# Performance work log

Measured on AMD Instinct MI355X. Metric: run time of the kernel, lower is better.

Reference implementation:

```python
import jax, jax.numpy as jnp
import numpy as np

ATT_K = 180   # attention_k
NPOOL = 15    # WeldonPooling(15): mean of top-15 + mean of bottom-15 spatial scores


def setup_inputs() -> dict:
    key = jax.random.key(0)
    k1, k2, k3, k4 = jax.random.split(key, 4)
    imgs, emb, h, w = 16, 2400, 14, 14
    caps_cnt = 64
    return {
        "g": jax.random.normal(k1, (imgs, emb, h, w), dtype=jnp.float32),
        "caps": jax.random.normal(k2, (caps_cnt, emb), dtype=jnp.float32),
        "fc_w": jax.random.normal(k3, (emb, emb), dtype=jnp.float32) * 0.02,
        "fc_b": jax.random.normal(k4, (emb,), dtype=jnp.float32) * 0.02,
    }


def reference(g, caps, fc_w, fc_b):
    imgs, emb, h, w = g.shape
    caps_cnt = caps.shape[0]

    # ---- WeldonPooling(15): per (img, channel) sort spatial scores ----
    flat = g.reshape(imgs, emb, h * w)
    s = jnp.sort(flat, axis=2)  # ascending
    hpool = s[:, :, -NPOOL:].mean(axis=2) + s[:, :, :NPOOL].mean(axis=2)  # [imgs, emb]
    x = hpool @ fc_w.T + fc_b  # fc (dropout is identity at eval / p=0)

    # ---- get_heat_map: top-k caption dims, gather fc-projected features ----
    order = jnp.argsort(-caps, axis=1)[:, :ATT_K]                 # [C, k] indices
    vals = jnp.take_along_axis(caps, order, axis=1)               # [C, k] top-k values (desc)
    gf = jnp.einsum('oe,iehw->oihw', fc_w, g)                     # fc.weight @ g -> [emb, imgs, h, w]
    gsel = gf[order]                                              # gather -> [C, k, imgs, h, w]
    heat = jnp.sum(jnp.abs(gsel * vals[:, :, None, None, None]), axis=1)  # [C, imgs, h, w]
    heat = jnp.transpose(heat, (1, 0, 2, 3))                      # [imgs, C, h, w]
    heat = heat / jnp.sum(heat, axis=(2, 3), keepdims=True)       # normalize per (img, cap)

    # ---- attention_embedding: weighted spatial sum, then fc ----
    xa = jnp.einsum('ichw,iehw->ice', heat, g)                    # [imgs, C, emb]
    xa = xa @ fc_w.T + fc_b

    return x, xa, g
```

## Files before the change

### kernel.cpp

```cpp
#include <hip/hip_runtime.h>
#include <math.h>

#define IMGS 16
#define EMB 2400
#define HW 196
#define CAPS 64
#define ATTK 180
#define NPOOL 15
#define NCOLS (IMGS * HW)
#define KPAD 224

typedef __attribute__((ext_vector_type(8))) short short8;
typedef __attribute__((ext_vector_type(4))) float f32x4;
typedef const __attribute__((address_space(1))) unsigned int* gas1_t;
typedef __attribute__((address_space(3))) unsigned int* las3_t;
typedef unsigned long long ull;

__device__ inline unsigned short f2bf(float f) {
    unsigned int u = __builtin_bit_cast(unsigned int, f);
    u += 0x7fffu + ((u >> 16) & 1u);
    return (unsigned short)(u >> 16);
}
__device__ inline float bf2f(unsigned int lo16) {
    return __builtin_bit_cast(float, lo16 << 16);
}
__device__ inline unsigned f2sort(float f) {
    unsigned u = __builtin_bit_cast(unsigned, f);
    int msk = ((int)u) >> 31;
    return u ^ (unsigned)(msk | 0x80000000);
}


__device__ __forceinline__ void transpool_body(char* smem, int bx, int i,
                                               const float* __restrict__ g,
                                               float* __restrict__ hpool,
                                               unsigned short* __restrict__ gT,
                                               float* __restrict__ gout) {
    float(*t)[197] = (float(*)[197])smem;
    int e0 = bx * 32;
    int tid = threadIdx.x;
    const float* base = g + ((size_t)i * EMB + e0) * HW;
    float* obase = gout ? gout + ((size_t)i * EMB + e0) * HW : nullptr;
    for (int f = tid; f < 32 * HW; f += 256) {
        int e = f / HW, hw = f % HW;
        float v = base[(size_t)e * HW + hw];
        t[e][hw] = v;
        if (obase) obase[(size_t)e * HW + hw] = v;
    }
    __syncthreads();
    for (int f = tid; f < HW * 32; f += 256) {
        int hw = f / 32, e = f % 32;
        gT[((size_t)i * HW + hw) * EMB + e0 + e] = f2bf(t[e][hw]);
    }
    int w = tid >> 6, tl = tid & 63, hl = tl & 31;
    bool negh = tl >= 32;
#pragma unroll 1
    for (int rr = 0; rr < 8; ++rr) {
        int e = w * 8 + rr;
        float s[7];
#pragma unroll
        for (int q = 0; q < 7; q++) {
            int hw = hl + 32 * q;
            if (hw < HW) {
                unsigned u = __builtin_bit_cast(unsigned, t[e][hw]);
                if (negh) u ^= 0x80000000u;
                u = (u & 0xFFFFFF00u) | (unsigned)(q * 32 + hl);
                s[q] = __builtin_bit_cast(float, u);
            } else {
                s[q] = -INFINITY;
            }
        }
#define CS(a, b)                                   \
    {                                              \
        float hi = fmaxf(s[a], s[b]);              \
        float lo = fminf(s[a], s[b]);              \
        s[a] = hi; s[b] = lo;                      \
    }
        CS(1, 2) CS(3, 4) CS(5, 6)
        CS(0, 2) CS(3, 5) CS(4, 6)
        CS(0, 1) CS(4, 5) CS(2, 6)
        CS(0, 4) CS(1, 5)
        CS(0, 3) CS(2, 5)
        CS(1, 3) CS(2, 4)
        CS(2, 3)
#undef CS
        float acc = 0.f;
#pragma unroll
        for (int it = 0; it < NPOOL; ++it) {
            int x = __builtin_bit_cast(int, s[0]);
#define ST(c)                                                                  \
    {                                                                          \
        int y = __builtin_amdgcn_update_dpp(x, x, c, 0xf, 0xf, false);         \
        float a = fmaxf(__builtin_bit_cast(float, x), __builtin_bit_cast(float, y)); \
        x = __builtin_bit_cast(int, a);                                        \
    }
            ST(0x111) ST(0x112) ST(0x114) ST(0x118) ST(0x142)
#undef ST
            int m31 = __builtin_amdgcn_readlane(x, 31);
            int m63 = __builtin_amdgcn_readlane(x, 63);
            float msel = __builtin_bit_cast(float, negh ? m63 : m31);
            acc += msel;
            bool won = (__builtin_bit_cast(unsigned, s[0]) ==
                        __builtin_bit_cast(unsigned, msel));
            s[0] = won ? s[1] : s[0];
            s[1] = won ? s[2] : s[1];
            s[2] = won ? s[3] : s[2];
            s[3] = won ? s[4] : s[3];
            s[4] = won ? s[5] : s[4];
            s[5] = won ? s[6] : s[5];
            s[6] = won ? -INFINITY : s[6];
        }
        int ai = __builtin_bit_cast(int, acc);
        float a0 = __builtin_bit_cast(float, __builtin_amdgcn_readlane(ai, 0));
        float a32 = __builtin_bit_cast(float, __builtin_amdgcn_readlane(ai, 32));
        if (tl == 0) hpool[(size_t)i * EMB + e0 + e] = (a0 - a32) / 15.0f;
    }
}

__device__ __forceinline__ void topk_body(char* smem, int c,
                                          const float* __restrict__ caps,
                                          int* __restrict__ idxs,
                                          float* __restrict__ vals) {
    float* rowf = (float*)smem;
    unsigned(*hist)[256] = (unsigned(*)[256])(smem + 9600);
    unsigned* scanbuf = (unsigned*)(smem + 13696);
    unsigned* wtot = (unsigned*)(smem + 14720);
    ull* sprefix = (ull*)(smem + 14744);
    int* srank = (int*)(smem + 14752);
    int tid = threadIdx.x;
    int w = tid >> 6, lane = tid & 63;
    const float4* src = (const float4*)(caps + (size_t)c * EMB);
    for (int j = tid; j < EMB / 4; j += 256) {
        float4 v = src[j];
        *(float4*)&rowf[j * 4] = v;
    }
    if (tid == 0) { *sprefix = 0ull; *srank = ATTK; }
#pragma unroll 1
    for (int pass = 0; pass < 6; ++pass) {
        __syncthreads();
        ull pref = *sprefix;
        int rk = *srank;
        int shift = 40 - pass * 8;
        ull pmaskhi = (pass == 0) ? 0ull : ~((1ull << (shift + 8)) - 1ull);
        hist[0][tid] = 0; hist[1][tid] = 0; hist[2][tid] = 0; hist[3][tid] = 0;
        __syncthreads();
        unsigned* myhist = hist[w];
#pragma unroll 1
        for (int s = 0; s < 10; s++) {
            int e = tid + s * 256;
            if (e < EMB) {
                ull key = ((ull)f2sort(rowf[e]) << 16) | ((unsigned)(2399 - e) << 4);
                if ((key & pmaskhi) == pref)
                    atomicAdd(&myhist[(unsigned)(key >> shift) & 255u], 1u);
            }
        }
        __syncthreads();
        unsigned h = hist[0][tid] + hist[1][tid] + hist[2][tid] + hist[3][tid];
        scanbuf[255 - tid] = h;
        __syncthreads();
        unsigned x = scanbuf[tid];
#pragma unroll
        for (int d = 1; d < 64; d <<= 1) {
            unsigned u = __shfl_up(x, d, 64);
            if (lane >= d) x += u;
        }
        if (lane == 63) wtot[w] = x;
        __syncthreads();
        unsigned off = 0;
        for (int ww = 0; ww < w; ww++) off += wtot[ww];
        scanbuf[tid] = x + off;
        __syncthreads();
        unsigned incl = scanbuf[255 - tid];
        unsigned excl = incl - h;
        if (h > 0u && excl < (unsigned)rk && incl >= (unsigned)rk) {
            *srank = rk - (int)excl;
            *sprefix = pref | ((ull)tid << shift);
        }
    }
    __syncthreads();
    ull T = *sprefix;
    unsigned selmask = 0, cnt = 0;
#pragma unroll 1
    for (int s = 0; s < 10; s++) {
        int e = tid + s * 256;
        if (e < EMB) {
            ull key = ((ull)f2sort(rowf[e]) << 16) | ((unsigned)(2399 - e) << 4);
            if (key >= T) { selmask |= 1u << s; cnt++; }
        }
    }
    unsigned x = cnt;
#pragma unroll
    for (int d = 1; d < 64; d <<= 1) {
        unsigned u = __shfl_up(x, d, 64);
        if (lane >= d) x += u;
    }
    if (lane == 63) wtot[w] = x;
    __syncthreads();
    unsigned off = 0;
    for (int ww = 0; ww < w; ww++) off += wtot[ww];
    unsigned slot = x + off - cnt;
#pragma unroll 1
    for (int s = 0; s < 10; s++) {
        if (selmask & (1u << s)) {
            int e = tid + s * 256;
            idxs[c * ATTK + slot] = e;
            vals[c * ATTK + slot] = fabsf(rowf[e]);
            slot++;
        }
    }
}

__device__ __forceinline__ void convw_body(int b, const float* __restrict__ fc_w,
                                           unsigned short* __restrict__ wbf) {
    int o = b * 4 + (threadIdx.x >> 6);
    int lane = threadIdx.x & 63;
    const float* wrow = fc_w + (size_t)o * EMB;
    unsigned short* wdst = wbf + (size_t)o * EMB;
    for (int e = lane * 4; e < EMB; e += 256) {
        float4 wv = *(const float4*)&wrow[e];
        ushort4 r;
        r.x = f2bf(wv.x); r.y = f2bf(wv.y); r.z = f2bf(wv.z); r.w = f2bf(wv.w);
        *(ushort4*)&wdst[e] = r;
    }
}

__global__ __launch_bounds__(256) void combo_kernel(const float* __restrict__ g,
                                                    float* __restrict__ hpool,
                                                    unsigned short* __restrict__ gT,
                                                    float* __restrict__ gout,
                                                    const float* __restrict__ caps,
                                                    int* __restrict__ idxs,
                                                    float* __restrict__ vals,
                                                    const float* __restrict__ fc_w,
                                                    unsigned short* __restrict__ wbf,
                                                    int nconv) {
    __shared__ __align__(16) char smem[25664];
    int b = blockIdx.x;
    if (b < CAPS) {
        topk_body(smem, b, caps, idxs, vals);
    } else if (b < CAPS + nconv) {
        convw_body(b - CAPS, fc_w, wbf);
    } else {
        int tb = b - CAPS - nconv;
        transpool_body(smem, tb % (EMB / 32), tb / (EMB / 32), g, hpool, gT, gout);
    }
}

__global__ __launch_bounds__(256) void x_bf_kernel(const float* __restrict__ hpool,
                                                   const unsigned short* __restrict__ wbf,
                                                   const float* __restrict__ fc_b,
                                                   float* __restrict__ x_out) {
    int o = blockIdx.x * 4 + (threadIdx.x >> 6);
    int lane = threadIdx.x & 63;
    float acc[IMGS];
#pragma unroll
    for (int i = 0; i < IMGS; i++) acc[i] = 0.f;
    const unsigned short* wrow = wbf + (size_t)o * EMB;
    for (int e = lane * 4; e < EMB; e += 256) {
        ushort4 wq = *(const ushort4*)&wrow[e];
        float w0 = bf2f(wq.x), w1 = bf2f(wq.y), w2 = bf2f(wq.z), w3 = bf2f(wq.w);
#pragma unroll
        for (int i = 0; i < IMGS; i++) {
            const float* hp = hpool + i * EMB + e;
            acc[i] += hp[0] * w0 + hp[1] * w1 + hp[2] * w2 + hp[3] * w3;
        }
    }
#pragma unroll
    for (int i = 0; i < IMGS; i++) {
#pragma unroll
        for (int sdx = 32; sdx > 0; sdx >>= 1) acc[i] += __shfl_xor(acc[i], sdx, 64);
    }
    if (lane == 0) {
        float bo = fc_b[o];
#pragma unroll
        for (int i = 0; i < IMGS; i++) x_out[i * EMB + o] = acc[i] + bo;
    }
}

__global__ void x_kernel(const float* __restrict__ hpool, const float* __restrict__ fc_w,
                         const float* __restrict__ fc_b, float* __restrict__ x_out) {
    int o = blockIdx.x;
    int lane = threadIdx.x;
    float acc[IMGS];
#pragma unroll
    for (int i = 0; i < IMGS; i++) acc[i] = 0.f;
    const float* wrow = fc_w + (size_t)o * EMB;
    for (int e = lane; e < EMB; e += 64) {
        float wv = wrow[e];
#pragma unroll
        for (int i = 0; i < IMGS; i++) acc[i] += hpool[i * EMB + e] * wv;
    }
#pragma unroll
    for (int i = 0; i < IMGS; i++) {
#pragma unroll
        for (int sdx = 32; sdx > 0; sdx >>= 1) acc[i] += __shfl_xor(acc[i], sdx, 64);
    }
    if (lane == 0) {
        float bo = fc_b[o];
#pragma unroll
        for (int i = 0; i < IMGS; i++) x_out[i * EMB + o] = acc[i] + bo;
    }
}

template <int MF, int NF, int OUT_MODE>
__global__ __launch_bounds__(256) void gemm_gll(const unsigned short* __restrict__ A,
                                                const unsigned short* __restrict__ B,
                                                void* __restrict__ outp,
                                                const float* __restrict__ bias,
                                                const float* __restrict__ invS,
                                                int M, int N, int K, int ldb, int kper,
                                                long az, long bz) {
    constexpr int BM = MF * 32, BN = NF * 32;
    constexpr int ROWS = BM + BN;
    constexpr int RPAD = (ROWS + 63) & ~63;
    constexpr int NCALL = RPAD / 16;
    constexpr int LPW = NCALL / 4;
    __shared__ unsigned short lds[3][RPAD][32];
    int gx = gridDim.x, gy = gridDim.y;
    int nwg = gx * gy;
    int flat = blockIdx.y * gx + blockIdx.x;
    int qq = nwg >> 3, rr8 = nwg & 7;
    int xcd = flat & 7, idx = flat >> 3;
    int base = (xcd < rr8) ? xcd * (qq + 1) : rr8 * (qq + 1) + (xcd - rr8) * qq;
    int nf = base + idx;
    int m0 = (nf % gy) * BM;
    int n0 = (nf / gy) * BN;
    int z = blockIdx.z;
    const unsigned short* Ab = A + (size_t)z * az;
    const unsigned short* Bb = B + (size_t)z * bz;
    int kb = (az == 0 && bz == 0) ? z * kper : 0;
    int nt = kper / 32;
    int tid = threadIdx.x, w = tid >> 6, lane = tid & 63;
    int wm = (w >> 1) * (MF * 16), wn = (w & 1) * (NF * 16);
    int ln = lane & 15;
    int ks = (((lane >> 4) ^ ((lane >> 1) & 3))) * 8;
    int srow = lane >> 2;
    int skc = (((lane & 3) ^ ((lane >> 3) & 3))) * 8;

    auto STAGE = [&](int buf, int t) {
        int k0 = kb + t * 32;
#pragma unroll
        for (int j = 0; j < LPW; j++) {
            int jj = w + j * 4;
            int r = jj * 16 + srow;
            const unsigned short* src;
            if (r < BM) src = Ab + (size_t)(m0 + r) * K + k0 + skc;
            else if (r < ROWS) src = Bb + (size_t)(n0 + r - BM) * ldb + k0 + skc;
            else src = Ab + (size_t)m0 * K + k0 + skc;
            __builtin_amdgcn_global_load_lds((gas1_t)(const void*)src,
                                             (las3_t)(void*)&lds[buf][jj * 16][0], 16, 0, 0);
        }
    };

    STAGE(0, 0);
    if (nt > 1) STAGE(1, 1);
    f32x4 acc[MF][NF] = {};
    for (int t = 0; t < nt; ++t) {
        if (t + 1 < nt) {
            if constexpr (LPW == 4) asm volatile("s_waitcnt vmcnt(4) lgkmcnt(0)" ::: "memory");
            else if constexpr (LPW == 5) asm volatile("s_waitcnt vmcnt(5) lgkmcnt(0)" ::: "memory");
            else if constexpr (LPW == 6) asm volatile("s_waitcnt vmcnt(6) lgkmcnt(0)" ::: "memory");
            else asm volatile("s_waitcnt vmcnt(0) lgkmcnt(0)" ::: "memory");
        } else {
            asm volatile("s_waitcnt vmcnt(0) lgkmcnt(0)" ::: "memory");
        }
        __builtin_amdgcn_s_barrier();
        __builtin_amdgcn_sched_barrier(0);
        if (t + 2 < nt) STAGE((t + 2) % 3, t + 2);
        const unsigned short(*buf)[32] = lds[t % 3];
        short8 af[MF], bfv[NF];
#pragma unroll
        for (int mf = 0; mf < MF; mf++)
            af[mf] = *(const short8*)&buf[wm + mf * 16 + ln][ks];
#pragma unroll
        for (int nfi = 0; nfi < NF; nfi++)
            bfv[nfi] = *(const short8*)&buf[BM + wn + nfi * 16 + ln][ks];
        __builtin_amdgcn_s_setprio(1);
#pragma unroll
        for (int mf = 0; mf < MF; mf++)
#pragma unroll
            for (int nfi = 0; nfi < NF; nfi++)
                acc[mf][nfi] = __builtin_amdgcn_mfma_f32_16x16x32_bf16(af[mf], bfv[nfi],
                                                                       acc[mf][nfi], 0, 0, 0);
        __builtin_amdgcn_s_setprio(0);
    }
#pragma unroll
    for (int mf = 0; mf < MF; mf++) {
#pragma unroll
        for (int nfi = 0; nfi < NF; nfi++) {
#pragma unroll
            for (int rr = 0; rr < 4; rr++) {
                int row = m0 + wm + mf * 16 + (lane >> 4) * 4 + rr;
                int col = n0 + wn + nfi * 16 + ln;
                float v = acc[mf][nfi][rr];
                if (OUT_MODE == 6) {
                    ((unsigned short*)outp)[(size_t)row * N + col] = f2bf(v);
                } else if (OUT_MODE == 4) {
                    ((float*)outp)[((size_t)z * CAPS + row) * N + col] =
                        v * invS[z * CAPS + row] + bias[col];
                }
            }
        }
    }
}

__device__ inline uint4 load8(const unsigned short* p) { return *(const uint4*)p; }
__device__ inline uint4 load8(const float* p) {
    float4 a = *(const float4*)p;
    float4 b = *(const float4*)(p + 4);
    uint4 r;
    r.x = (unsigned)f2bf(a.x) | ((unsigned)f2bf(a.y) << 16);
    r.y = (unsigned)f2bf(a.z) | ((unsigned)f2bf(a.w) << 16);
    r.z = (unsigned)f2bf(b.x) | ((unsigned)f2bf(b.y) << 16);
    r.w = (unsigned)f2bf(b.z) | ((unsigned)f2bf(b.w) << 16);
    return r;
}

template <int MF, int NF, typename TA, typename TB>
__global__ __launch_bounds__(256) void mfma_gemm_nt(const TA* __restrict__ A,
                                                    const TB* __restrict__ B,
                                                    void* __restrict__ outp,
                                                    int M, int N, int K) {
    constexpr int BM = MF * 32, BN = NF * 32;
    constexpr int nA = BM * 4, nTot = (BM + BN) * 4;
    constexpr int NCH = (nTot + 255) / 256;
    __shared__ unsigned short As[BM][40];
    __shared__ unsigned short Bs[BN][40];
    int m0 = blockIdx.y * BM, n0 = blockIdx.x * BN;
    int tid = threadIdx.x;
    int w = tid >> 6, lane = tid & 63;
    int wm = (w >> 1) * (MF * 16), wn = (w & 1) * (NF * 16);
    int ln = lane & 15, ks = (lane >> 4) * 8;
    uint4 r[NCH];
#pragma unroll
    for (int j = 0; j < NCH; j++) {
        int c = tid + 256 * j;
        if (c < nTot) {
            if (c < nA) {
                int row = c >> 2, kc = c & 3;
                r[j] = load8(A + (size_t)(m0 + row) * K + kc * 8);
            } else {
                int cc = c - nA, row = cc >> 2, kc = cc & 3;
                r[j] = load8(B + (size_t)(n0 + row) * K + kc * 8);
            }
        }
    }
    f32x4 acc[MF][NF] = {};
    for (int k0 = 0; k0 < K; k0 += 32) {
#pragma unroll
        for (int j = 0; j < NCH; j++) {
            int c = tid + 256 * j;
            if (c < nTot) {
                if (c < nA) {
                    int row = c >> 2, kc = c & 3;
                    *(uint4*)&As[row][kc * 8] = r[j];
                } else {
                    int cc = c - nA, row = cc >> 2, kc = cc & 3;
                    *(uint4*)&Bs[row][kc * 8] = r[j];
                }
            }
        }
        __syncthreads();
        if (k0 + 32 < K) {
#pragma unroll
            for (int j = 0; j < NCH; j++) {
                int c = tid + 256 * j;
                if (c < nTot) {
                    if (c < nA) {
                        int row = c >> 2, kc = c & 3;
                        r[j] = load8(A + (size_t)(m0 + row) * K + (k0 + 32) + kc * 8);
                    } else {
                        int cc = c - nA, row = cc >> 2, kc = cc & 3;
                        r[j] = load8(B + (size_t)(n0 + row) * K + (k0 + 32) + kc * 8);
                    }
                }
            }
        }
        short8 af[MF], bfv[NF];
#pragma unroll
        for (int mf = 0; mf < MF; mf++)
            af[mf] = *(const short8*)&As[wm + mf * 16 + ln][ks];
#pragma unroll
        for (int nfi = 0; nfi < NF; nfi++)
            bfv[nfi] = *(const short8*)&Bs[wn + nfi * 16 + ln][ks];
#pragma unroll
        for (int mf = 0; mf < MF; mf++)
#pragma unroll
            for (int nfi = 0; nfi < NF; nfi++)
                acc[mf][nfi] = __builtin_amdgcn_mfma_f32_16x16x32_bf16(af[mf], bfv[nfi],
                                                                       acc[mf][nfi], 0, 0, 0);
        __syncthreads();
    }
#pragma unroll
    for (int mf = 0; mf < MF; mf++) {
#pragma unroll
        for (int nfi = 0; nfi < NF; nfi++) {
#pragma unroll
            for (int rr = 0; rr < 4; rr++) {
                int row = m0 + wm + mf * 16 + (lane >> 4) * 4 + rr;
                int col = n0 + wn + nfi * 16 + ln;
                ((unsigned short*)outp)[(size_t)row * N + col] = f2bf(acc[mf][nfi][rr]);
            }
        }
    }
}

__global__ __launch_bounds__(256) void heat_kernel(const int* __restrict__ idxs,
                                                   const float* __restrict__ vals,
                                                   const unsigned short* __restrict__ A,
                                                   unsigned short* __restrict__ Hnbf,
                                                   float* __restrict__ invS) {
    __shared__ int sidx[ATTK];
    __shared__ float sval[ATTK];
    __shared__ float wsum[4];
    int i = blockIdx.x, c = blockIdx.y;
    int tid = threadIdx.x;
    int w = tid >> 6, lane = tid & 63;
    if (tid < ATTK) {
        sidx[tid] = idxs[c * ATTK + tid];
        sval[tid] = vals[c * ATTK + tid];
    }
    __syncthreads();
    int hw = tid;
    float v = 0.f;
    if (hw < HW) {
        int n = i * HW + hw;
        float a0 = 0.f, a1 = 0.f, a2 = 0.f, a3 = 0.f;
#pragma unroll 1
        for (int j = 0; j < ATTK; j += 4) {
            a0 += sval[j + 0] * bf2f(A[(size_t)sidx[j + 0] * NCOLS + n] & 0x7FFFu);
            a1 += sval[j + 1] * bf2f(A[(size_t)sidx[j + 1] * NCOLS + n] & 0x7FFFu);
            a2 += sval[j + 2] * bf2f(A[(size_t)sidx[j + 2] * NCOLS + n] & 0x7FFFu);
            a3 += sval[j + 3] * bf2f(A[(size_t)sidx[j + 3] * NCOLS + n] & 0x7FFFu);
        }
        v = (a0 + a1) + (a2 + a3);
    }
    if (hw < KPAD)
        Hnbf[((size_t)i * CAPS + c) * KPAD + hw] = (hw < HW) ? f2bf(v) : (unsigned short)0;
    float s = v;
#pragma unroll
    for (int d = 32; d > 0; d >>= 1) s += __shfl_xor(s, d, 64);
    if (lane == 0) wsum[w] = s;
    __syncthreads();
    if (tid == 0)
        invS[i * CAPS + c] = 1.0f / (wsum[0] + wsum[1] + wsum[2] + wsum[3]);
}

extern "C" void kernel_launch(void* const* d_in, const int* in_sizes, int n_in,
                              void* d_out, int out_size, void* d_ws, size_t ws_size,
                              hipStream_t stream) {
    const float* g = (const float*)d_in[0];
    const float* caps = (const float*)d_in[1];
    const float* fc_w = (const float*)d_in[2];
    const float* fc_b = (const float*)d_in[3];

    float* out = (float*)d_out;
    float* x_out = out;
    float* xa_out = out + 38400;
    float* g_out = out + 38400 + 2457600;

    float* ws = (float*)d_ws;
    float* hpool = ws;
    int* idxs = (int*)(ws + 38400);
    float* vals = ws + 49920;
    float* invS = ws + 61440;
    unsigned short* Hnbf = (unsigned short*)(ws + 62464);
    unsigned short* wbf = (unsigned short*)(ws + 1490944);
    bool use_wbf = ws_size >= (size_t)17483776;
    bool ws_big = use_wbf && ws_size >= (size_t)(17483776 + 2 * 15052800);
    unsigned short* gT_big = (unsigned short*)((char*)d_ws + 17483776);
    unsigned short* Asig_big = (unsigned short*)((char*)d_ws + 17483776 + 15052800);

    unsigned short* Asig = ws_big ? Asig_big : (unsigned short*)g_out;
    unsigned short* gT = ws_big ? gT_big : ((unsigned short*)g_out + (size_t)EMB * NCOLS);

    if (use_wbf) {
        combo_kernel<<<CAPS + EMB / 4 + (EMB / 32) * IMGS, 256, 0, stream>>>(
            g, hpool, gT, ws_big ? g_out : nullptr, caps, idxs, vals, fc_w, wbf, EMB / 4);
        x_bf_kernel<<<EMB / 4, 256, 0, stream>>>(hpool, wbf, fc_b, x_out);
        gemm_gll<5, 7, 6><<<dim3(NCOLS / 224, EMB / 160, 1), 256, 0, stream>>>(
            wbf, gT, Asig, nullptr, nullptr, EMB, NCOLS, EMB, EMB, EMB, 0, 0);
    } else {
        combo_kernel<<<CAPS + (EMB / 32) * IMGS, 256, 0, stream>>>(
            g, hpool, gT, nullptr, caps, idxs, vals, fc_w, nullptr, 0);
        x_kernel<<<EMB, 64, 0, stream>>>(hpool, fc_w, fc_b, x_out);
        mfma_gemm_nt<5, 2, float, unsigned short>
            <<<dim3(NCOLS / 64, EMB / 160), 256, 0, stream>>>(fc_w, gT, Asig,
                                                              EMB, NCOLS, EMB);
    }
    heat_kernel<<<dim3(IMGS, CAPS), 256, 0, stream>>>(idxs, vals, Asig, Hnbf, invS);
    gemm_gll<2, 5, 4><<<dim3(EMB / 160, 1, IMGS), 256, 0, stream>>>(
        Hnbf, Asig, xa_out, fc_b, invS, CAPS, EMB, KPAD, NCOLS, KPAD,
        (long)CAPS * KPAD, HW);
    if (!ws_big) {
        hipMemcpyAsync(g_out, g, sizeof(float) * (size_t)IMGS * EMB * HW,
                       hipMemcpyDeviceToDevice, stream);
    }
}
```

Baseline: 151.5 us.

## Batch Weldon pooling over four rows, fuse x projection into heat kernel

The pooling loop now processes four channel rows at once, interleaving their DPP max reductions to expose instruction-level parallelism. The combo kernel block order is changed so the heavy transpose/pool blocks are scheduled first and top-k blocks last. The separate x projection kernel is removed and its blocks are appended to the heat kernel launch, cutting one launch and letting it overlap with heat work. The cost is higher register pressure from the four-row state in the pooling body.

```diff
diff --git a/kernel.cpp b/kernel.cpp
--- a/kernel.cpp
+++ b/kernel.cpp
@@ -55,65 +55,81 @@
     int w = tid >> 6, tl = tid & 63, hl = tl & 31;
     bool negh = tl >= 32;
 #pragma unroll 1
-    for (int rr = 0; rr < 8; ++rr) {
-        int e = w * 8 + rr;
-        float s[7];
-#pragma unroll
-        for (int q = 0; q < 7; q++) {
-            int hw = hl + 32 * q;
-            if (hw < HW) {
-                unsigned u = __builtin_bit_cast(unsigned, t[e][hw]);
-                if (negh) u ^= 0x80000000u;
-                u = (u & 0xFFFFFF00u) | (unsigned)(q * 32 + hl);
-                s[q] = __builtin_bit_cast(float, u);
-            } else {
-                s[q] = -INFINITY;
-            }
-        }
-#define CS(a, b)                                   \
-    {                                              \
-        float hi = fmaxf(s[a], s[b]);              \
-        float lo = fminf(s[a], s[b]);              \
-        s[a] = hi; s[b] = lo;                      \
-    }
-        CS(1, 2) CS(3, 4) CS(5, 6)
-        CS(0, 2) CS(3, 5) CS(4, 6)
-        CS(0, 1) CS(4, 5) CS(2, 6)
-        CS(0, 4) CS(1, 5)
-        CS(0, 3) CS(2, 5)
-        CS(1, 3) CS(2, 4)
-        CS(2, 3)
-#undef CS
-        float acc = 0.f;
+    for (int rq = 0; rq < 2; ++rq) {
+        int eb = w * 8 + rq * 4;
+        float s[4][7];
+#pragma unroll
+        for (int r = 0; r < 4; r++) {
+#pragma unroll
+            for (int q = 0; q < 7; q++) {
+                int hw = hl + 32 * q;
+                if (hw < HW) {
+                    unsigned u = __builtin_bit_cast(unsigned, t[eb + r][hw]);
+                    if (negh) u ^= 0x80000000u;
+                    s[r][q] = __builtin_bit_cast(
+                        float, (u & 0xFFFFFF00u) | (unsigned)(q * 32 + hl));
+                } else {
+                    s[r][q] = -INFINITY;
+                }
+            }
+        }
+#define CS1(r, a, b)                                       \
+    {                                                      \
+        float hi = fmaxf(s[r][a], s[r][b]);                \
+        float lo = fminf(s[r][a], s[r][b]);                \
+        s[r][a] = hi; s[r][b] = lo;                        \
+    }
+#define CSQ(a, b) CS1(0, a, b) CS1(1, a, b) CS1(2, a, b) CS1(3, a, b)
+        CSQ(1, 2) CSQ(3, 4) CSQ(5, 6)
+        CSQ(0, 2) CSQ(3, 5) CSQ(4, 6)
+        CSQ(0, 1) CSQ(4, 5) CSQ(2, 6)
+        CSQ(0, 4) CSQ(1, 5)
+        CSQ(0, 3) CSQ(2, 5)
+        CSQ(1, 3) CSQ(2, 4)
+        CSQ(2, 3)
+#undef CSQ
+#undef CS1
+        float acc[4] = {0.f, 0.f, 0.f, 0.f};
 #pragma unroll
         for (int it = 0; it < NPOOL; ++it) {
-            int x = __builtin_bit_cast(int, s[0]);
-#define ST(c)                                                                  \
-    {                                                                          \
-        int y = __builtin_amdgcn_update_dpp(x, x, c, 0xf, 0xf, false);         \
-        float a = fmaxf(__builtin_bit_cast(float, x), __builtin_bit_cast(float, y)); \
-        x = __builtin_bit_cast(int, a);                                        \
-    }
-            ST(0x111) ST(0x112) ST(0x114) ST(0x118) ST(0x142)
-#undef ST
-            int m31 = __builtin_amdgcn_readlane(x, 31);
-            int m63 = __builtin_amdgcn_readlane(x, 63);
-            float msel = __builtin_bit_cast(float, negh ? m63 : m31);
-            acc += msel;
-            bool won = (__builtin_bit_cast(unsigned, s[0]) ==
-                        __builtin_bit_cast(unsigned, msel));
-            s[0] = won ? s[1] : s[0];
-            s[1] = won ? s[2] : s[1];
-            s[2] = won ? s[3] : s[2];
-            s[3] = won ? s[4] : s[3];
-            s[4] = won ? s[5] : s[4];
-            s[5] = won ? s[6] : s[5];
-            s[6] = won ? -INFINITY : s[6];
-        }
-        int ai = __builtin_bit_cast(int, acc);
-        float a0 = __builtin_bit_cast(float, __builtin_amdgcn_readlane(ai, 0));
-        float a32 = __builtin_bit_cast(float, __builtin_amdgcn_readlane(ai, 32));
-        if (tl == 0) hpool[(size_t)i * EMB + e0 + e] = (a0 - a32) / 15.0f;
+            int xx[4];
+#pragma unroll
+            for (int r = 0; r < 4; r++) xx[r] = __builtin_bit_cast(int, s[r][0]);
+#define ST4(c)                                                                     \
+    {                                                                              \
+        _Pragma("unroll") for (int r = 0; r < 4; r++) {                            \
+            int y = __builtin_amdgcn_update_dpp(xx[r], xx[r], c, 0xf, 0xf, false); \
+            float a = fmaxf(__builtin_bit_cast(float, xx[r]),                      \
+                            __builtin_bit_cast(float, y));                         \
+            xx[r] = __builtin_bit_cast(int, a);                                    \
+        }                                                                          \
+    }
+            ST4(0x111) ST4(0x112) ST4(0x114) ST4(0x118) ST4(0x142)
+#undef ST4
+#pragma unroll
+            for (int r = 0; r < 4; r++) {
+                int m31 = __builtin_amdgcn_readlane(xx[r], 31);
+                int m63 = __builtin_amdgcn_readlane(xx[r], 63);
+                float msel = __builtin_bit_cast(float, negh ? m63 : m31);
+                acc[r] += msel;
+                bool won = (__builtin_bit_cast(unsigned, s[r][0]) ==
+                            __builtin_bit_cast(unsigned, msel));
+                s[r][0] = won ? s[r][1] : s[r][0];
+                s[r][1] = won ? s[r][2] : s[r][1];
+                s[r][2] = won ? s[r][3] : s[r][2];
+                s[r][3] = won ? s[r][4] : s[r][3];
+                s[r][4] = won ? s[r][5] : s[r][4];
+                s[r][5] = won ? s[r][6] : s[r][5];
+                s[r][6] = won ? -INFINITY : s[r][6];
+            }
+        }
+#pragma unroll
+        for (int r = 0; r < 4; r++) {
+            int ai = __builtin_bit_cast(int, acc[r]);
+            float a0 = __builtin_bit_cast(float, __builtin_amdgcn_readlane(ai, 0));
+            float a32 = __builtin_bit_cast(float, __builtin_amdgcn_readlane(ai, 32));
+            if (tl == 0) hpool[(size_t)i * EMB + e0 + eb + r] = (a0 - a32) / 15.0f;
+        }
     }
 }
 
@@ -236,44 +252,13 @@
                                                     int nconv) {
     __shared__ __align__(16) char smem[25664];
     int b = blockIdx.x;
-    if (b < CAPS) {
-        topk_body(smem, b, caps, idxs, vals);
-    } else if (b < CAPS + nconv) {
-        convw_body(b - CAPS, fc_w, wbf);
+    constexpr int NTP = (EMB / 32) * IMGS;
+    if (b < NTP) {
+        transpool_body(smem, b % (EMB / 32), b / (EMB / 32), g, hpool, gT, gout);
+    } else if (b < NTP + nconv) {
+        convw_body(b - NTP, fc_w, wbf);
     } else {
-        int tb = b - CAPS - nconv;
-        transpool_body(smem, tb % (EMB / 32), tb / (EMB / 32), g, hpool, gT, gout);
-    }
-}
-
-__global__ __launch_bounds__(256) void x_bf_kernel(const float* __restrict__ hpool,
-                                                   const unsigned short* __restrict__ wbf,
-                                                   const float* __restrict__ fc_b,
-                                                   float* __restrict__ x_out) {
-    int o = blockIdx.x * 4 + (threadIdx.x >> 6);
-    int lane = threadIdx.x & 63;
-    float acc[IMGS];
-#pragma unroll
-    for (int i = 0; i < IMGS; i++) acc[i] = 0.f;
-    const unsigned short* wrow = wbf + (size_t)o * EMB;
-    for (int e = lane * 4; e < EMB; e += 256) {
-        ushort4 wq = *(const ushort4*)&wrow[e];
-        float w0 = bf2f(wq.x), w1 = bf2f(wq.y), w2 = bf2f(wq.z), w3 = bf2f(wq.w);
-#pragma unroll
-        for (int i = 0; i < IMGS; i++) {
-            const float* hp = hpool + i * EMB + e;
-            acc[i] += hp[0] * w0 + hp[1] * w1 + hp[2] * w2 + hp[3] * w3;
-        }
-    }
-#pragma unroll
-    for (int i = 0; i < IMGS; i++) {
-#pragma unroll
-        for (int sdx = 32; sdx > 0; sdx >>= 1) acc[i] += __shfl_xor(acc[i], sdx, 64);
-    }
-    if (lane == 0) {
-        float bo = fc_b[o];
-#pragma unroll
-        for (int i = 0; i < IMGS; i++) x_out[i * EMB + o] = acc[i] + bo;
+        topk_body(smem, b - NTP - nconv, caps, idxs, vals);
     }
 }
 
@@ -505,45 +490,79 @@
     }
 }
 
-__global__ __launch_bounds__(256) void heat_kernel(const int* __restrict__ idxs,
-                                                   const float* __restrict__ vals,
-                                                   const unsigned short* __restrict__ A,
-                                                   unsigned short* __restrict__ Hnbf,
-                                                   float* __restrict__ invS) {
+__global__ __launch_bounds__(256) void heatx_kernel(const int* __restrict__ idxs,
+                                                    const float* __restrict__ vals,
+                                                    const unsigned short* __restrict__ A,
+                                                    unsigned short* __restrict__ Hnbf,
+                                                    float* __restrict__ invS,
+                                                    const float* __restrict__ hpool,
+                                                    const unsigned short* __restrict__ wbf,
+                                                    const float* __restrict__ fc_b,
+                                                    float* __restrict__ x_out,
+                                                    int nheat) {
     __shared__ int sidx[ATTK];
     __shared__ float sval[ATTK];
     __shared__ float wsum[4];
-    int i = blockIdx.x, c = blockIdx.y;
+    int b = blockIdx.x;
     int tid = threadIdx.x;
     int w = tid >> 6, lane = tid & 63;
-    if (tid < ATTK) {
-        sidx[tid] = idxs[c * ATTK + tid];
-        sval[tid] = vals[c * ATTK + tid];
-    }
-    __syncthreads();
-    int hw = tid;
-    float v = 0.f;
-    if (hw < HW) {
-        int n = i * HW + hw;
-        float a0 = 0.f, a1 = 0.f, a2 = 0.f, a3 = 0.f;
+    if (b < nheat) {
+        int i = b % IMGS, c = b / IMGS;
+        if (tid < ATTK) {
+            sidx[tid] = idxs[c * ATTK + tid];
+            sval[tid] = vals[c * ATTK + tid];
+        }
+        __syncthreads();
+        int hw = tid;
+        float v = 0.f;
+        if (hw < HW) {
+            int n = i * HW + hw;
+            float a0 = 0.f, a1 = 0.f, a2 = 0.f, a3 = 0.f;
 #pragma unroll 1
-        for (int j = 0; j < ATTK; j += 4) {
-            a0 += sval[j + 0] * bf2f(A[(size_t)sidx[j + 0] * NCOLS + n] & 0x7FFFu);
-            a1 += sval[j + 1] * bf2f(A[(size_t)sidx[j + 1] * NCOLS + n] & 0x7FFFu);
-            a2 += sval[j + 2] * bf2f(A[(size_t)sidx[j + 2] * NCOLS + n] & 0x7FFFu);
-            a3 += sval[j + 3] * bf2f(A[(size_t)sidx[j + 3] * NCOLS + n] & 0x7FFFu);
-        }
-        v = (a0 + a1) + (a2 + a3);
-    }
-    if (hw < KPAD)
-        Hnbf[((size_t)i * CAPS + c) * KPAD + hw] = (hw < HW) ? f2bf(v) : (unsigned short)0;
-    float s = v;
-#pragma unroll
-    for (int d = 32; d > 0; d >>= 1) s += __shfl_xor(s, d, 64);
-    if (lane == 0) wsum[w] = s;
-    __syncthreads();
-    if (tid == 0)
-        invS[i * CAPS + c] = 1.0f / (wsum[0] + wsum[1] + wsum[2] + wsum[3]);
+            for (int j = 0; j < ATTK; j += 4) {
+                a0 += sval[j + 0] * bf2f(A[(size_t)sidx[j + 0] * NCOLS + n] & 0x7FFFu);
+                a1 += sval[j + 1] * bf2f(A[(size_t)sidx[j + 1] * NCOLS + n] & 0x7FFFu);
+                a2 += sval[j + 2] * bf2f(A[(size_t)sidx[j + 2] * NCOLS + n] & 0x7FFFu);
+                a3 += sval[j + 3] * bf2f(A[(size_t)sidx[j + 3] * NCOLS + n] & 0x7FFFu);
+            }
+            v = (a0 + a1) + (a2 + a3);
+        }
+        if (hw < KPAD)
+            Hnbf[((size_t)i * CAPS + c) * KPAD + hw] =
+                (hw < HW) ? f2bf(v) : (unsigned short)0;
+        float s = v;
+#pragma unroll
+        for (int d = 32; d > 0; d >>= 1) s += __shfl_xor(s, d, 64);
+        if (lane == 0) wsum[w] = s;
+        __syncthreads();
+        if (tid == 0)
+            invS[i * CAPS + c] = 1.0f / (wsum[0] + wsum[1] + wsum[2] + wsum[3]);
+    } else {
+        int o = (b - nheat) * 4 + w;
+        float acc[IMGS];
+#pragma unroll
+        for (int i = 0; i < IMGS; i++) acc[i] = 0.f;
+        const unsigned short* wrow = wbf + (size_t)o * EMB;
+        for (int e = lane * 4; e < EMB; e += 256) {
+            ushort4 wq = *(const ushort4*)&wrow[e];
+            float w0 = bf2f(wq.x), w1 = bf2f(wq.y), w2 = bf2f(wq.z), w3 = bf2f(wq.w);
+#pragma unroll
+            for (int i = 0; i < IMGS; i++) {
+                const float* hp = hpool + i * EMB + e;
+                acc[i] += hp[0] * w0 + hp[1] * w1 + hp[2] * w2 + hp[3] * w3;
+            }
+        }
+#pragma unroll
+        for (int i = 0; i < IMGS; i++) {
+#pragma unroll
+            for (int sdx = 32; sdx > 0; sdx >>= 1) acc[i] += __shfl_xor(acc[i], sdx, 64);
+        }
+        if (lane == 0) {
+            float bo = fc_b[o];
+#pragma unroll
+            for (int i = 0; i < IMGS; i++) x_out[i * EMB + o] = acc[i] + bo;
+        }
+    }
 }
 
 extern "C" void kernel_launch(void* const* d_in, const int* in_sizes, int n_in,
@@ -575,20 +594,22 @@
     unsigned short* gT = ws_big ? gT_big : ((unsigned short*)g_out + (size_t)EMB * NCOLS);
 
     if (use_wbf) {
-        combo_kernel<<<CAPS + EMB / 4 + (EMB / 32) * IMGS, 256, 0, stream>>>(
+        combo_kernel<<<(EMB / 32) * IMGS + EMB / 4 + CAPS, 256, 0, stream>>>(
             g, hpool, gT, ws_big ? g_out : nullptr, caps, idxs, vals, fc_w, wbf, EMB / 4);
-        x_bf_kernel<<<EMB / 4, 256, 0, stream>>>(hpool, wbf, fc_b, x_out);
         gemm_gll<5, 7, 6><<<dim3(NCOLS / 224, EMB / 160, 1), 256, 0, stream>>>(
             wbf, gT, Asig, nullptr, nullptr, EMB, NCOLS, EMB, EMB, EMB, 0, 0);
+        heatx_kernel<<<IMGS * CAPS + EMB / 4, 256, 0, stream>>>(
+            idxs, vals, Asig, Hnbf, invS, hpool, wbf, fc_b, x_out, IMGS * CAPS);
     } else {
-        combo_kernel<<<CAPS + (EMB / 32) * IMGS, 256, 0, stream>>>(
+        combo_kernel<<<(EMB / 32) * IMGS + CAPS, 256, 0, stream>>>(
             g, hpool, gT, nullptr, caps, idxs, vals, fc_w, nullptr, 0);
         x_kernel<<<EMB, 64, 0, stream>>>(hpool, fc_w, fc_b, x_out);
         mfma_gemm_nt<5, 2, float, unsigned short>
             <<<dim3(NCOLS / 64, EMB / 160), 256, 0, stream>>>(fc_w, gT, Asig,
                                                               EMB, NCOLS, EMB);
-    }
-    heat_kernel<<<dim3(IMGS, CAPS), 256, 0, stream>>>(idxs, vals, Asig, Hnbf, invS);
+        heatx_kernel<<<IMGS * CAPS, 256, 0, stream>>>(
+            idxs, vals, Asig, Hnbf, invS, hpool, nullptr, fc_b, x_out, IMGS * CAPS);
+    }
     gemm_gll<2, 5, 4><<<dim3(EMB / 160, 1, IMGS), 256, 0, stream>>>(
         Hnbf, Asig, xa_out, fc_b, invS, CAPS, EMB, KPAD, NCOLS, KPAD,
         (long)CAPS * KPAD, HW);
```

Measured after the change: 147.0 us, median of 2. 1.03x faster.
